# Kernel optimization log

Measured on AMD Instinct MI355X. Metric: run time of the kernel, lower is better.

The kernel has to match this reference:

```python
import jax, jax.numpy as jnp
import numpy as np

B, C, N, K = 8, 192, 3136, 9
OUT_CH = 192
BN_EPS = 1e-5


def setup_inputs() -> dict:
    key = jax.random.key(0)
    k1, k2, k3, k4 = jax.random.split(key, 4)
    x = jax.random.normal(k1, (B, C, N, 1), dtype=jnp.float32)
    y = jax.random.normal(k2, (B, C, N, 1), dtype=jnp.float32)
    edge_index = jax.random.randint(k3, (2, B, N, K), 0, N, dtype=jnp.int64)
    # 1x1 conv weight (out_ch, in_ch*2), no bias (BatchNorm follows)
    W = jax.random.normal(k4, (OUT_CH, 2 * C), dtype=jnp.float32) / np.sqrt(2 * C)
    gamma = jnp.ones((OUT_CH,), dtype=jnp.float32)
    beta = jnp.zeros((OUT_CH,), dtype=jnp.float32)
    return {"x": x, "y": y, "edge_index": edge_index, "W": W, "gamma": gamma, "beta": beta}


def _gather(feat, idx):
    # feat: (B, C, N); idx: (B, M, K) -> (B, C, M, K)
    return jax.vmap(lambda f, i: f[:, i])(feat, idx)


def reference(x, y, edge_index, W, gamma, beta):
    xt = x[..., 0]  # (B, C, N)
    yt = y[..., 0]
    x_i = _gather(xt, edge_index[1])          # (B, C, N, K)
    x_j = _gather(yt, edge_index[0])          # (B, C, N, K)
    rel = jnp.max(x_j - x_i, axis=-1, keepdims=True)  # (B, C, N, 1)
    h = jnp.concatenate([x, rel], axis=1)     # (B, 2C, N, 1)
    # 1x1 conv
    out = jnp.einsum('oc,bcnk->bonk', W, h)   # (B, out_ch, N, 1)
    # BatchNorm2d (training-mode batch statistics)
    mean = out.mean(axis=(0, 2, 3), keepdims=True)
    var = out.var(axis=(0, 2, 3), keepdims=True)
    out = (out - mean) * jax.lax.rsqrt(var + BN_EPS)
    out = out * gamma[None, :, None, None] + beta[None, :, None, None]
    return jax.nn.gelu(out, approximate=False)
```

## Files before the change

kernel.cpp:

```cpp
#include <hip/hip_runtime.h>
#include <hip/hip_bf16.h>

#define B_    8
#define C_    192
#define N_    3136
#define K_    9
#define OC    192
#define KDIM  384
#define ROWS  (B_ * N_)
#define BNK   (B_ * N_ * K_)

typedef __hip_bfloat16 bf16;
using short8 = __attribute__((ext_vector_type(8))) short;
using us4    = __attribute__((ext_vector_type(4))) unsigned short;
using f32x4  = __attribute__((ext_vector_type(4))) float;

__device__ inline float bfbits2f(unsigned short u) {
    unsigned int x = ((unsigned int)u) << 16;
    return __builtin_bit_cast(float, x);
}
__device__ inline bf16 f2bf(float v) { return __float2bfloat16(v); }
__device__ inline unsigned short f2bfbits(float v) {
    bf16 t = __float2bfloat16(v);
    return *reinterpret_cast<unsigned short*>(&t);
}

__global__ void k_prep(const float* __restrict__ x, const float* __restrict__ y,
                       const float* __restrict__ W,
                       bf16* __restrict__ h, bf16* __restrict__ yT,
                       bf16* __restrict__ Wb, float* __restrict__ stats) {
    int tx = threadIdx.x, ty = threadIdx.y;
    int bz = blockIdx.z;
    if (bz == 16) {
        int flat = blockIdx.y * 98 + blockIdx.x;
        int t = ty * 32 + tx;
        if (flat < 288) {
            int i = flat * 256 + t;
            Wb[i] = f2bf(W[i]);
        }
        if (flat == 0) stats[t] = 0.f;
        if (flat == 1 && t < 128) stats[256 + t] = 0.f;
        return;
    }
    __shared__ float tile[32][33];
    int n0 = blockIdx.x * 32, c0 = blockIdx.y * 32;
    int b = bz >> 1, which = bz & 1;
    const float* src = which ? y : x;
#pragma unroll
    for (int i = 0; i < 4; i++) {
        int c = c0 + ty + i * 8;
        tile[ty + i * 8][tx] = src[((size_t)b * C_ + c) * N_ + n0 + tx];
    }
    __syncthreads();
    if (which == 0) {
#pragma unroll
        for (int i = 0; i < 4; i++) {
            int n = n0 + ty + i * 8;
            h[((size_t)b * N_ + n) * KDIM + c0 + tx] = f2bf(tile[tx][ty + i * 8]);
        }
    } else {
#pragma unroll
        for (int i = 0; i < 4; i++) {
            int n = n0 + ty + i * 8;
            yT[((size_t)b * N_ + n) * C_ + c0 + tx] = f2bf(tile[tx][ty + i * 8]);
        }
    }
}

__global__ void k_gather_rel(const int* __restrict__ ei, bf16* __restrict__ h,
                             const bf16* __restrict__ yT) {
    int wave = threadIdx.x >> 6;
    int lane = threadIdx.x & 63;
    int r = blockIdx.x * 4 + wave;
    int b = r / N_;

    const int* e0 = ei + (size_t)r * K_;
    const int* e1 = ei + (size_t)BNK + (size_t)r * K_;
    int ej[K_], eii[K_];
#pragma unroll
    for (int k = 0; k < K_; k++) { ej[k] = e0[k]; eii[k] = e1[k]; }

    const us4* y4 = (const us4*)(yT + (size_t)b * N_ * C_);
    const us4* x4 = (const us4*)(h + (size_t)b * N_ * KDIM);

    if (lane < 48) {
        float m0 = -3.4e38f, m1 = -3.4e38f, m2 = -3.4e38f, m3 = -3.4e38f;
#pragma unroll
        for (int k = 0; k < K_; k++) {
            us4 vy = y4[(size_t)ej[k] * 48 + lane];
            us4 vx = x4[(size_t)eii[k] * 96 + lane];
            m0 = fmaxf(m0, bfbits2f(vy.x) - bfbits2f(vx.x));
            m1 = fmaxf(m1, bfbits2f(vy.y) - bfbits2f(vx.y));
            m2 = fmaxf(m2, bfbits2f(vy.z) - bfbits2f(vx.z));
            m3 = fmaxf(m3, bfbits2f(vy.w) - bfbits2f(vx.w));
        }
        us4 o;
        o.x = f2bfbits(m0); o.y = f2bfbits(m1);
        o.z = f2bfbits(m2); o.w = f2bfbits(m3);
        *((us4*)(h + (size_t)r * KDIM + C_) + lane) = o;
    }
}

__launch_bounds__(192)
__global__ void k_gemm_stats(const bf16* __restrict__ h, const bf16* __restrict__ Wb,
                             float* __restrict__ stats) {
    int tid = threadIdx.x;
    int wave = tid >> 6, lane = tid & 63;
    int fcol = lane & 15, fgrp = lane >> 4;
    int r0 = blockIdx.x * 64;
    int colbase = wave * 64;

    f32x4 acc[4][4] = {};

    for (int kk = 0; kk < 12; kk++) {
        short8 a[4], bb[4];
#pragma unroll
        for (int i = 0; i < 4; i++)
            a[i] = *reinterpret_cast<const short8*>(
                h + (size_t)(r0 + i * 16 + fcol) * KDIM + kk * 32 + fgrp * 8);
#pragma unroll
        for (int j = 0; j < 4; j++)
            bb[j] = *reinterpret_cast<const short8*>(
                Wb + (size_t)(colbase + j * 16 + fcol) * KDIM + kk * 32 + fgrp * 8);
#pragma unroll
        for (int i = 0; i < 4; i++)
#pragma unroll
            for (int j = 0; j < 4; j++)
                acc[i][j] = __builtin_amdgcn_mfma_f32_16x16x32_bf16(a[i], bb[j], acc[i][j], 0, 0, 0);
    }

#pragma unroll
    for (int j = 0; j < 4; j++) {
        int o = colbase + j * 16 + fcol;
        float s1 = 0.f, s2 = 0.f;
#pragma unroll
        for (int i = 0; i < 4; i++)
#pragma unroll
            for (int e = 0; e < 4; e++) {
                float v = acc[i][j][e];
                s1 += v;
                s2 += v * v;
            }
        s1 += __shfl_xor(s1, 16); s1 += __shfl_xor(s1, 32);
        s2 += __shfl_xor(s2, 16); s2 += __shfl_xor(s2, 32);
        if (fgrp == 0) {
            atomicAdd(&stats[o], s1);
            atomicAdd(&stats[OC + o], s2);
        }
    }
}

__launch_bounds__(192)
__global__ void k_gemm_bn(const bf16* __restrict__ h, const bf16* __restrict__ Wb,
                          const float* __restrict__ stats,
                          const float* __restrict__ gamma, const float* __restrict__ beta,
                          float* __restrict__ out) {
    int tid = threadIdx.x;
    int wave = tid >> 6, lane = tid & 63;
    int fcol = lane & 15, fgrp = lane >> 4;
    int r0 = blockIdx.x * 64;
    int b = r0 / N_;
    int n0 = r0 % N_;
    int colbase = wave * 64;

    f32x4 acc[4][4] = {};

    for (int kk = 0; kk < 12; kk++) {
        short8 wfr[4], hfr[4];
#pragma unroll
        for (int i = 0; i < 4; i++)
            wfr[i] = *reinterpret_cast<const short8*>(
                Wb + (size_t)(colbase + i * 16 + fcol) * KDIM + kk * 32 + fgrp * 8);
#pragma unroll
        for (int j = 0; j < 4; j++)
            hfr[j] = *reinterpret_cast<const short8*>(
                h + (size_t)(r0 + j * 16 + fcol) * KDIM + kk * 32 + fgrp * 8);
#pragma unroll
        for (int i = 0; i < 4; i++)
#pragma unroll
            for (int j = 0; j < 4; j++)
                acc[i][j] = __builtin_amdgcn_mfma_f32_16x16x32_bf16(wfr[i], hfr[j], acc[i][j], 0, 0, 0);
    }

    const float invc = 1.0f / (float)ROWS;
#pragma unroll
    for (int i = 0; i < 4; i++) {
#pragma unroll
        for (int e = 0; e < 4; e++) {
            int o = colbase + i * 16 + fgrp * 4 + e;
            float mean = stats[o] * invc;
            float var  = stats[OC + o] * invc - mean * mean;
            float is   = rsqrtf(var + 1e-5f);
            float sc = gamma[o] * is;
            float sh = beta[o] - mean * sc;
#pragma unroll
            for (int j = 0; j < 4; j++) {
                float z = acc[i][j][e] * sc + sh;
                float gl = 0.5f * z * (1.0f + erff(z * 0.70710678118654752f));
                out[((size_t)b * OC + o) * N_ + n0 + j * 16 + fcol] = gl;
            }
        }
    }
}

extern "C" void kernel_launch(void* const* d_in, const int* in_sizes, int n_in,
                              void* d_out, int out_size, void* d_ws, size_t ws_size,
                              hipStream_t stream) {
    const float* x     = (const float*)d_in[0];
    const float* y     = (const float*)d_in[1];
    const int*   ei    = (const int*)d_in[2];
    const float* W     = (const float*)d_in[3];
    const float* gamma = (const float*)d_in[4];
    const float* beta  = (const float*)d_in[5];
    float* out = (float*)d_out;

    char* ws = (char*)d_ws;
    bf16*  h     = (bf16*)(ws);
    bf16*  yT    = (bf16*)(ws + 19267584);
    bf16*  Wb    = (bf16*)(ws + 19267584 + 9633792);
    float* stats = (float*)(ws + 19267584 + 9633792 + 147456);

    dim3 bt(32, 8);
    k_prep<<<dim3(N_ / 32, C_ / 32, 2 * B_ + 1), bt, 0, stream>>>(x, y, W, h, yT, Wb, stats);
    k_gather_rel<<<ROWS / 4, 256, 0, stream>>>(ei, h, yT);
    k_gemm_stats<<<ROWS / 64, 192, 0, stream>>>(h, Wb, stats);
    k_gemm_bn<<<ROWS / 64, 192, 0, stream>>>(h, Wb, stats, gamma, beta, out);
}
```

Baseline: 166.4 us.

## Fuse neighbor gather-max into the stats GEMM kernel

```diff
diff --git a/kernel.cpp b/kernel.cpp
--- a/kernel.cpp
+++ b/kernel.cpp
@@ -67,85 +67,87 @@
     }
 }
 
-__global__ void k_gather_rel(const int* __restrict__ ei, bf16* __restrict__ h,
-                             const bf16* __restrict__ yT) {
-    int wave = threadIdx.x >> 6;
-    int lane = threadIdx.x & 63;
-    int r = blockIdx.x * 4 + wave;
-    int b = r / N_;
-
-    const int* e0 = ei + (size_t)r * K_;
-    const int* e1 = ei + (size_t)BNK + (size_t)r * K_;
-    int ej[K_], eii[K_];
-#pragma unroll
-    for (int k = 0; k < K_; k++) { ej[k] = e0[k]; eii[k] = e1[k]; }
-
-    const us4* y4 = (const us4*)(yT + (size_t)b * N_ * C_);
-    const us4* x4 = (const us4*)(h + (size_t)b * N_ * KDIM);
-
-    if (lane < 48) {
-        float m0 = -3.4e38f, m1 = -3.4e38f, m2 = -3.4e38f, m3 = -3.4e38f;
-#pragma unroll
-        for (int k = 0; k < K_; k++) {
-            us4 vy = y4[(size_t)ej[k] * 48 + lane];
-            us4 vx = x4[(size_t)eii[k] * 96 + lane];
-            m0 = fmaxf(m0, bfbits2f(vy.x) - bfbits2f(vx.x));
-            m1 = fmaxf(m1, bfbits2f(vy.y) - bfbits2f(vx.y));
-            m2 = fmaxf(m2, bfbits2f(vy.z) - bfbits2f(vx.z));
-            m3 = fmaxf(m3, bfbits2f(vy.w) - bfbits2f(vx.w));
-        }
-        us4 o;
-        o.x = f2bfbits(m0); o.y = f2bfbits(m1);
-        o.z = f2bfbits(m2); o.w = f2bfbits(m3);
-        *((us4*)(h + (size_t)r * KDIM + C_) + lane) = o;
-    }
-}
-
-__launch_bounds__(192)
-__global__ void k_gemm_stats(const bf16* __restrict__ h, const bf16* __restrict__ Wb,
-                             float* __restrict__ stats) {
-    int tid = threadIdx.x;
-    int wave = tid >> 6, lane = tid & 63;
-    int fcol = lane & 15, fgrp = lane >> 4;
-    int r0 = blockIdx.x * 64;
-    int colbase = wave * 64;
-
-    f32x4 acc[4][4] = {};
-
-    for (int kk = 0; kk < 12; kk++) {
-        short8 a[4], bb[4];
-#pragma unroll
-        for (int i = 0; i < 4; i++)
-            a[i] = *reinterpret_cast<const short8*>(
-                h + (size_t)(r0 + i * 16 + fcol) * KDIM + kk * 32 + fgrp * 8);
-#pragma unroll
-        for (int j = 0; j < 4; j++)
-            bb[j] = *reinterpret_cast<const short8*>(
-                Wb + (size_t)(colbase + j * 16 + fcol) * KDIM + kk * 32 + fgrp * 8);
-#pragma unroll
-        for (int i = 0; i < 4; i++)
-#pragma unroll
-            for (int j = 0; j < 4; j++)
-                acc[i][j] = __builtin_amdgcn_mfma_f32_16x16x32_bf16(a[i], bb[j], acc[i][j], 0, 0, 0);
-    }
-
-#pragma unroll
-    for (int j = 0; j < 4; j++) {
-        int o = colbase + j * 16 + fcol;
-        float s1 = 0.f, s2 = 0.f;
-#pragma unroll
-        for (int i = 0; i < 4; i++)
-#pragma unroll
-            for (int e = 0; e < 4; e++) {
-                float v = acc[i][j][e];
-                s1 += v;
-                s2 += v * v;
+__launch_bounds__(256)
+__global__ void k_gather_stats(const int* __restrict__ ei, bf16* __restrict__ h,
+                               const bf16* __restrict__ yT,
+                               const bf16* __restrict__ Wb,
+                               float* __restrict__ stats) {
+    const int tid = threadIdx.x;
+    const int wave = tid >> 6, lane = tid & 63;
+    const int r0 = blockIdx.x * 64;
+
+    {
+        const int rbase = r0 + wave * 16;
+        for (int rr = 0; rr < 16; rr++) {
+            int r = rbase + rr;
+            int bb = r / N_;
+            const int* e0 = ei + (size_t)r * K_;
+            const int* e1 = ei + (size_t)BNK + (size_t)r * K_;
+            int ej[K_], ex[K_];
+#pragma unroll
+            for (int k = 0; k < K_; k++) { ej[k] = e0[k]; ex[k] = e1[k]; }
+
+            const us4* y4 = (const us4*)(yT + (size_t)bb * N_ * C_);
+            const us4* x4 = (const us4*)(h + (size_t)bb * N_ * KDIM);
+
+            if (lane < 48) {
+                float m0 = -3.4e38f, m1 = -3.4e38f, m2 = -3.4e38f, m3 = -3.4e38f;
+#pragma unroll
+                for (int k = 0; k < K_; k++) {
+                    us4 vy = y4[(size_t)ej[k] * 48 + lane];
+                    us4 vx = x4[(size_t)ex[k] * 96 + lane];
+                    m0 = fmaxf(m0, bfbits2f(vy.x) - bfbits2f(vx.x));
+                    m1 = fmaxf(m1, bfbits2f(vy.y) - bfbits2f(vx.y));
+                    m2 = fmaxf(m2, bfbits2f(vy.z) - bfbits2f(vx.z));
+                    m3 = fmaxf(m3, bfbits2f(vy.w) - bfbits2f(vx.w));
+                }
+                us4 o;
+                o.x = f2bfbits(m0); o.y = f2bfbits(m1);
+                o.z = f2bfbits(m2); o.w = f2bfbits(m3);
+                *((us4*)(h + (size_t)r * KDIM + C_) + lane) = o;
             }
-        s1 += __shfl_xor(s1, 16); s1 += __shfl_xor(s1, 32);
-        s2 += __shfl_xor(s2, 16); s2 += __shfl_xor(s2, 32);
-        if (fgrp == 0) {
-            atomicAdd(&stats[o], s1);
-            atomicAdd(&stats[OC + o], s2);
+        }
+    }
+    __syncthreads();
+
+    {
+        const int fcol = lane & 15, fgrp = lane >> 4;
+        const int colbase = wave * 48;
+        f32x4 acc[4][3] = {};
+        for (int kk = 0; kk < 12; kk++) {
+            short8 a[4], bb[3];
+#pragma unroll
+            for (int i = 0; i < 4; i++)
+                a[i] = *reinterpret_cast<const short8*>(
+                    h + (size_t)(r0 + i * 16 + fcol) * KDIM + kk * 32 + fgrp * 8);
+#pragma unroll
+            for (int j = 0; j < 3; j++)
+                bb[j] = *reinterpret_cast<const short8*>(
+                    Wb + (size_t)(colbase + j * 16 + fcol) * KDIM + kk * 32 + fgrp * 8);
+#pragma unroll
+            for (int i = 0; i < 4; i++)
+#pragma unroll
+                for (int j = 0; j < 3; j++)
+                    acc[i][j] = __builtin_amdgcn_mfma_f32_16x16x32_bf16(a[i], bb[j], acc[i][j], 0, 0, 0);
+        }
+#pragma unroll
+        for (int j = 0; j < 3; j++) {
+            int o = colbase + j * 16 + fcol;
+            float s1 = 0.f, s2 = 0.f;
+#pragma unroll
+            for (int i = 0; i < 4; i++)
+#pragma unroll
+                for (int e = 0; e < 4; e++) {
+                    float v = acc[i][j][e];
+                    s1 += v;
+                    s2 += v * v;
+                }
+            s1 += __shfl_xor(s1, 16); s1 += __shfl_xor(s1, 32);
+            s2 += __shfl_xor(s2, 16); s2 += __shfl_xor(s2, 32);
+            if (fgrp == 0) {
+                atomicAdd(&stats[o], s1);
+                atomicAdd(&stats[OC + o], s2);
+            }
         }
     }
 }
@@ -222,7 +224,6 @@
 
     dim3 bt(32, 8);
     k_prep<<<dim3(N_ / 32, C_ / 32, 2 * B_ + 1), bt, 0, stream>>>(x, y, W, h, yT, Wb, stats);
-    k_gather_rel<<<ROWS / 4, 256, 0, stream>>>(ei, h, yT);
-    k_gemm_stats<<<ROWS / 64, 192, 0, stream>>>(h, Wb, stats);
+    k_gather_stats<<<ROWS / 64, 256, 0, stream>>>(ei, h, yT, Wb, stats);
     k_gemm_bn<<<ROWS / 64, 192, 0, stream>>>(h, Wb, stats, gamma, beta, out);
 }
```

After: 174.3 us. 4.8% more time.
